# Performance work log

Hardware: AMD Instinct MI355X
Metric: run time of the kernel (lower is better)

The kernel has to match this reference:

```python
import jax, jax.numpy as jnp
import numpy as np

# Event marker constants (PASS/MAP both trigger map writes, STEP triggers step writes)
PASS, MAP, STEP = 0, 1, 2
GRAPH_STEPS = 3
B, T, D, K, V = 64, 12, 256, 256, 512
S = 2 * K  # num_symbols


def gelu(x):
    return jax.nn.gelu(x, approximate=False)  # torch nn.GELU default = exact erf


def mlp2(x, W1, b1, W2, b2):
    return gelu(x @ W1 + b1) @ W2 + b2


def setup_inputs() -> dict:
    key = jax.random.key(0)
    ks = jax.random.split(key, 32)

    def lin(k, fan_in, shape):
        return (jax.random.normal(k, shape, dtype=jnp.float32) / np.float32(np.sqrt(fan_in)))

    return {
        "event_marker": jax.random.randint(ks[0], (B, T), 0, 3),
        "source_idx": jax.random.randint(ks[1], (B, T), 0, S),
        "source_valid": jax.random.randint(ks[2], (B, T), 0, 2),
        "target_symbol_idx": jax.random.randint(ks[3], (B, T), 0, S),
        "target_symbol_valid": jax.random.randint(ks[4], (B, T), 0, 2),
        "target_value_idx": jax.random.randint(ks[5], (B, T), 0, V),
        "target_value_valid": jax.random.randint(ks[6], (B, T), 0, 2),
        "query_idx": jax.random.randint(ks[7], (B,), 0, S),
        "query_valid": jax.random.randint(ks[8], (B,), 0, 2),
        "evidence": jax.random.normal(ks[9], (B, T, D), dtype=jnp.float32),
        "symbol_emb": jax.random.normal(ks[10], (S, D), dtype=jnp.float32) * 0.02,
        "value_emb": jax.random.normal(ks[11], (V, D), dtype=jnp.float32) * 0.02,
        "Wmg1": lin(ks[12], D, (D, D)), "bmg1": jnp.zeros((D,), jnp.float32),
        "Wmg2": lin(ks[13], D, (D, 1)), "bmg2": jnp.zeros((1,), jnp.float32),
        "Wsg1": lin(ks[14], D, (D, D)), "bsg1": jnp.zeros((D,), jnp.float32),
        "Wsg2": lin(ks[15], D, (D, 1)), "bsg2": jnp.zeros((1,), jnp.float32),
        "Wf1": lin(ks[16], 2 * D, (2 * D, D)), "bf1": jnp.zeros((D,), jnp.float32),
        "Wf2": lin(ks[17], D, (D, D)), "bf2": jnp.zeros((D,), jnp.float32),
        "Wo1": lin(ks[18], 2 * D, (2 * D, D)), "bo1": jnp.zeros((D,), jnp.float32),
        "Wo2": lin(ks[19], D, (D, V)), "bo2": jnp.zeros((V,), jnp.float32),
    }


def reference(event_marker, source_idx, source_valid, target_symbol_idx,
              target_symbol_valid, target_value_idx, target_value_valid,
              query_idx, query_valid, evidence, symbol_emb, value_emb,
              Wmg1, bmg1, Wmg2, bmg2, Wsg1, bsg1, Wsg2, bsg2,
              Wf1, bf1, Wf2, bf2, Wo1, bo1, Wo2, bo2):
    f32 = evidence.dtype
    brange = jnp.arange(B)

    # --- TypedGraphMemory.update, applied over T sequential events ---
    # one-hot outer-product write  ==  scatter-add of gated scalar at (b, src, tgt)
    def step(carry, ev):
        map_mem, step_mem = carry
        marker, src, sv, tsym, tsv, tval, tvv, evd = ev
        mg = jax.nn.sigmoid(mlp2(evd, Wmg1, bmg1, Wmg2, bmg2))[:, 0]  # [B]
        sg = jax.nn.sigmoid(mlp2(evd, Wsg1, bsg1, Wsg2, bsg2))[:, 0]  # [B]
        map_mask = (((marker == PASS) | (marker == MAP)) & (sv > 0) & (tvv > 0)).astype(f32)
        step_mask = ((marker == STEP) & (sv > 0) & (tsv > 0)).astype(f32)
        src_c = jnp.clip(src, 0, S - 1)
        tsym_c = jnp.clip(tsym, 0, S - 1)
        tval_c = jnp.clip(tval, 0, V - 1)
        map_mem = map_mem.at[brange, src_c, tval_c].add(mg * map_mask)
        step_mem = step_mem.at[brange, src_c, tsym_c].add(sg * step_mask)
        return (map_mem, step_mem), None

    ev_seq = (event_marker.T, source_idx.T, source_valid.T, target_symbol_idx.T,
              target_symbol_valid.T, target_value_idx.T, target_value_valid.T,
              jnp.swapaxes(evidence, 0, 1))  # time-major
    init = (jnp.zeros((B, S, V), f32), jnp.zeros((B, S, S), f32))
    (map_mem, step_mem), _ = jax.lax.scan(step, init, ev_seq)

    # --- TypedGraphMemory.query_readout ---
    walk = jax.nn.one_hot(jnp.clip(query_idx, 0, S - 1), S, dtype=f32)
    walk = walk * query_valid.astype(f32)[:, None]
    acc_v = jnp.einsum('bs,bsv->bv', walk, map_mem)   # [B,V]
    acc_s = walk @ symbol_emb                         # [B,D]
    for _ in range(GRAPH_STEPS):
        walk = jnp.einsum('bs,bst->bt', walk, step_mem)
        acc_v = acc_v + jnp.einsum('bs,bsv->bv', walk, map_mem)
        acc_s = acc_s + walk @ symbol_emb
    graph_state = jnp.concatenate([acc_s, acc_v @ value_emb], axis=-1)  # [B,2D]
    logits = mlp2(graph_state, Wo1, bo1, Wo2, bo2)      # [B,V]
    feedback = mlp2(graph_state, Wf1, bf1, Wf2, bf2)    # [B,D]
    return logits, feedback
```

## Files before the change

### kernel.cpp

```cpp
#include <hip/hip_runtime.h>
#include <math.h>

#define NB 64
#define NT 12
#define ND 256
#define NS 512
#define NV 512

__device__ __forceinline__ float gelu_exact(float x) {
    return 0.5f * x * (1.0f + erff(x * 0.70710678118654752f));
}
__device__ __forceinline__ float sigmoidf_(float x) {
    return 1.0f / (1.0f + __expf(-x));
}

__global__ __launch_bounds__(512) void k_gates_readout(
    const int* __restrict__ marker, const int* __restrict__ srci,
    const int* __restrict__ srcv, const int* __restrict__ tsymi,
    const int* __restrict__ tsymv, const int* __restrict__ tvali,
    const int* __restrict__ tvalv, const int* __restrict__ qidx,
    const int* __restrict__ qvld,
    const float* __restrict__ evidence,
    const float* __restrict__ symbol_emb, const float* __restrict__ value_emb,
    const float* __restrict__ Wmg1, const float* __restrict__ bmg1,
    const float* __restrict__ Wmg2, const float* __restrict__ bmg2,
    const float* __restrict__ Wsg1, const float* __restrict__ bsg1,
    const float* __restrict__ Wsg2, const float* __restrict__ bsg2,
    float* __restrict__ gs)
{
    const int b = blockIdx.x, tid = threadIdx.x;
    const int g = tid >> 8;
    const int j = tid & 255;
    const int lane = tid & 63, wv = tid >> 6;

    __shared__ float red[8][NT];
    __shared__ float gate_s[2][NT];

    {
        const float* __restrict__ W1 = g ? Wsg1 : Wmg1;
        const float* __restrict__ b1 = g ? bsg1 : bmg1;
        const float* __restrict__ W2 = g ? Wsg2 : Wmg2;
        const float* __restrict__ ev = evidence + b * (NT * ND);

        float h[NT];
        #pragma unroll
        for (int t = 0; t < NT; ++t) h[t] = 0.0f;

        #pragma unroll 8
        for (int i = 0; i < ND; ++i) {
            float w = W1[i * ND + j];
            #pragma unroll
            for (int t = 0; t < NT; ++t) h[t] += ev[t * ND + i] * w;
        }

        const float b1j = b1[j], w2j = W2[j];
        #pragma unroll
        for (int t = 0; t < NT; ++t) {
            float v = gelu_exact(h[t] + b1j) * w2j;
            #pragma unroll
            for (int off = 32; off > 0; off >>= 1) v += __shfl_down(v, off, 64);
            if (lane == 0) red[wv][t] = v;
        }
    }
    __syncthreads();
    if (tid < 24) {
        int gg = tid / NT, tt = tid - gg * NT;
        float s = red[gg * 4 + 0][tt] + red[gg * 4 + 1][tt] +
                  red[gg * 4 + 2][tt] + red[gg * 4 + 3][tt] +
                  (gg ? bsg2[0] : bmg2[0]);
        gate_s[gg][tt] = sigmoidf_(s);
    }

    __shared__ float walk[NS], nxt[NS];
    __shared__ int   esrc[NT], etsym[NT], etval[NT];
    __shared__ float mapw[NT], stepw[NT];
    __shared__ int   sidx[64]; __shared__ float sval[64];
    __shared__ int   vidx[64]; __shared__ float vval[64];
    __shared__ int   scnt, vcnt;

    walk[tid] = 0.f; nxt[tid] = 0.f;
    if (tid == 0) { scnt = 0; vcnt = 0; }
    if (tid >= 256 && tid < 256 + NT) {
        int t = tid - 256;
        int e = b * NT + t;
        int mk = marker[e];
        int sv_ = srcv[e], tsv_ = tsymv[e], tvv_ = tvalv[e];
        esrc[t]  = min(max(srci[e], 0), NS - 1);
        etsym[t] = min(max(tsymi[e], 0), NS - 1);
        etval[t] = min(max(tvali[e], 0), NV - 1);
        mapw[t]  = (((mk == 0) || (mk == 1)) && (sv_ > 0) && (tvv_ > 0)) ? 1.f : 0.f;
        stepw[t] = ((mk == 2) && (sv_ > 0) && (tsv_ > 0)) ? 1.f : 0.f;
    }
    __syncthreads();
    if (tid < NT) {
        mapw[tid]  *= gate_s[0][tid];
        stepw[tid] *= gate_s[1][tid];
    }
    if (tid == 256) {
        int qc = min(max(qidx[b], 0), NS - 1);
        float qv = (float)qvld[b];
        walk[qc] = qv;
        if (qv != 0.f) { sidx[0] = qc; sval[0] = qv; scnt = 1; }
    }
    __syncthreads();
    if (tid < NT) {
        float c = walk[esrc[tid]] * mapw[tid];
        if (c != 0.f) { int k = atomicAdd(&vcnt, 1); vidx[k] = etval[tid]; vval[k] = c; }
    }
    __syncthreads();
    for (int stp = 0; stp < 3; ++stp) {
        if (tid < NT) {
            float c = walk[esrc[tid]] * stepw[tid];
            if (c != 0.f) {
                atomicAdd(&nxt[etsym[tid]], c);
                int k = atomicAdd(&scnt, 1); sidx[k] = etsym[tid]; sval[k] = c;
            }
        }
        __syncthreads();
        { float a = nxt[tid]; walk[tid] = a; nxt[tid] = 0.f; }
        __syncthreads();
        if (tid < NT) {
            float c = walk[esrc[tid]] * mapw[tid];
            if (c != 0.f) { int k = atomicAdd(&vcnt, 1); vidx[k] = etval[tid]; vval[k] = c; }
        }
        __syncthreads();
    }
    const int d = tid & 255;
    const float* __restrict__ emb  = (tid < 256) ? symbol_emb : value_emb;
    const int*   idxl = (tid < 256) ? sidx : vidx;
    const float* vall = (tid < 256) ? sval : vval;
    const int n = (tid < 256) ? scnt : vcnt;
    float acc = 0.f;
    int k = 0;
    for (; k + 4 <= n; k += 4) {
        int   i0 = idxl[k],     i1 = idxl[k + 1], i2 = idxl[k + 2], i3 = idxl[k + 3];
        float w0 = vall[k],     w1 = vall[k + 1], w2 = vall[k + 2], w3 = vall[k + 3];
        float r0 = emb[i0 * ND + d], r1 = emb[i1 * ND + d];
        float r2 = emb[i2 * ND + d], r3 = emb[i3 * ND + d];
        acc += w0 * r0; acc += w1 * r1; acc += w2 * r2; acc += w3 * r3;
    }
    for (; k < n; ++k) acc += vall[k] * emb[idxl[k] * ND + d];
    gs[b * 512 + (tid < 256 ? 0 : 256) + d] = acc;
}

__global__ __launch_bounds__(512) void k_mlp1(
    const float* __restrict__ gs,
    const float* __restrict__ Wo1, const float* __restrict__ bo1,
    const float* __restrict__ Wf1, const float* __restrict__ bf1,
    float* __restrict__ H)
{
    const int blk = blockIdx.x;
    const int m = blk >> 5;
    const int r = blk & 31;
    const int js = r >> 3, bt = r & 7;
    const int tid = threadIdx.x;
    const int lane = tid & 63;
    const int bsub = (tid >> 6) & 3;
    const int ih = tid >> 8;
    const int j = js * 64 + lane;
    const int b0 = bt * 8 + bsub * 2, b1_ = b0 + 1;

    const float* __restrict__ W1   = (m ? Wf1 : Wo1) + ih * 256 * 256;
    const float* __restrict__ bias = m ? bf1 : bo1;
    const float* __restrict__ x0 = gs + b0 * 512 + ih * 256;
    const float* __restrict__ x1 = gs + b1_ * 512 + ih * 256;

    float a0 = 0.f, a1 = 0.f;
    #pragma unroll 8
    for (int i = 0; i < 256; ++i) {
        float w = W1[i * 256 + j];
        a0 += x0[i] * w; a1 += x1[i] * w;
    }
    __shared__ float part[256][2];
    if (ih == 1) { part[tid & 255][0] = a0; part[tid & 255][1] = a1; }
    __syncthreads();
    if (ih == 0) {
        float bj = bias[j];
        H[m * (NB * 256) + b0 * 256 + j]  = gelu_exact(a0 + part[tid][0] + bj);
        H[m * (NB * 256) + b1_ * 256 + j] = gelu_exact(a1 + part[tid][1] + bj);
    }
}

__global__ __launch_bounds__(512) void k_mlp2(
    const float* __restrict__ H,
    const float* __restrict__ Wo2, const float* __restrict__ bo2,
    const float* __restrict__ Wf2, const float* __restrict__ bf2,
    float* __restrict__ out)
{
    const int blk = blockIdx.x;
    const int tid = threadIdx.x;
    const int lane = tid & 63;
    const int bsub = (tid >> 6) & 3;
    const int ih = tid >> 8;
    __shared__ float part[256][2];

    if (blk < 64) {
        const int bt = blk >> 3, vs = blk & 7;
        const int v = vs * 64 + lane;
        const int b0 = bt * 8 + bsub * 2, b1_ = b0 + 1;
        const float* __restrict__ h0 = H + b0 * 256 + ih * 128;
        const float* __restrict__ h1 = H + b1_ * 256 + ih * 128;
        const float* __restrict__ Wp = Wo2 + ih * 128 * 512;
        float a0 = 0.f, a1 = 0.f;
        #pragma unroll 8
        for (int k = 0; k < 128; ++k) {
            float w = Wp[k * 512 + v];
            a0 += h0[k] * w; a1 += h1[k] * w;
        }
        if (ih == 1) { part[tid & 255][0] = a0; part[tid & 255][1] = a1; }
        __syncthreads();
        if (ih == 0) {
            float bv = bo2[v];
            out[b0 * 512 + v]  = a0 + part[tid][0] + bv;
            out[b1_ * 512 + v] = a1 + part[tid][1] + bv;
        }
    } else {
        const int r = blk - 64;
        const int bt = r >> 2, ds = r & 3;
        const int d = ds * 64 + lane;
        const int b0 = bt * 8 + bsub * 2, b1_ = b0 + 1;
        const float* __restrict__ h0 = H + (NB * 256) + b0 * 256 + ih * 128;
        const float* __restrict__ h1 = H + (NB * 256) + b1_ * 256 + ih * 128;
        const float* __restrict__ Wp = Wf2 + ih * 128 * 256;
        float a0 = 0.f, a1 = 0.f;
        #pragma unroll 8
        for (int k = 0; k < 128; ++k) {
            float w = Wp[k * 256 + d];
            a0 += h0[k] * w; a1 += h1[k] * w;
        }
        if (ih == 1) { part[tid & 255][0] = a0; part[tid & 255][1] = a1; }
        __syncthreads();
        if (ih == 0) {
            float bd = bf2[d];
            out[NB * NV + b0 * 256 + d]  = a0 + part[tid][0] + bd;
            out[NB * NV + b1_ * 256 + d] = a1 + part[tid][1] + bd;
        }
    }
}

extern "C" void kernel_launch(void* const* d_in, const int* in_sizes, int n_in,
                              void* d_out, int out_size, void* d_ws, size_t ws_size,
                              hipStream_t stream) {
    const int* event_marker       = (const int*)d_in[0];
    const int* source_idx         = (const int*)d_in[1];
    const int* source_valid       = (const int*)d_in[2];
    const int* target_symbol_idx  = (const int*)d_in[3];
    const int* target_symbol_vld  = (const int*)d_in[4];
    const int* target_value_idx   = (const int*)d_in[5];
    const int* target_value_vld   = (const int*)d_in[6];
    const int* query_idx          = (const int*)d_in[7];
    const int* query_valid        = (const int*)d_in[8];
    const float* evidence   = (const float*)d_in[9];
    const float* symbol_emb = (const float*)d_in[10];
    const float* value_emb  = (const float*)d_in[11];
    const float* Wmg1 = (const float*)d_in[12]; const float* bmg1 = (const float*)d_in[13];
    const float* Wmg2 = (const float*)d_in[14]; const float* bmg2 = (const float*)d_in[15];
    const float* Wsg1 = (const float*)d_in[16]; const float* bsg1 = (const float*)d_in[17];
    const float* Wsg2 = (const float*)d_in[18]; const float* bsg2 = (const float*)d_in[19];
    const float* Wf1  = (const float*)d_in[20]; const float* bf1  = (const float*)d_in[21];
    const float* Wf2  = (const float*)d_in[22]; const float* bf2  = (const float*)d_in[23];
    const float* Wo1  = (const float*)d_in[24]; const float* bo1  = (const float*)d_in[25];
    const float* Wo2  = (const float*)d_in[26]; const float* bo2  = (const float*)d_in[27];

    float* ws = (float*)d_ws;
    float* gs = ws;
    float* H  = ws + 32768;

    k_gates_readout<<<dim3(64), dim3(512), 0, stream>>>(
        event_marker, source_idx, source_valid, target_symbol_idx,
        target_symbol_vld, target_value_idx, target_value_vld,
        query_idx, query_valid, evidence, symbol_emb, value_emb,
        Wmg1, bmg1, Wmg2, bmg2, Wsg1, bsg1, Wsg2, bsg2, gs);
    k_mlp1<<<dim3(64), dim3(512), 0, stream>>>(gs, Wo1, bo1, Wf1, bf1, H);
    k_mlp2<<<dim3(96), dim3(512), 0, stream>>>(H, Wo2, bo2, Wf2, bf2, (float*)d_out);
}
```

Before: 164.0 us.

## Split gate MLP into separate wide-grid kernel before graph readout

Moves the gate MLP computation out of the per-batch readout kernel into its own kernel. The new kernel launches 256 blocks of 1024 threads, split by batch, gate type and time half, with a split-K reduction over the input dimension through shared memory. The aim is to fill far more compute units than the original 64 blocks and shorten the serial dot-product chain per thread. In exchange it adds an extra kernel launch and a global round trip for the gate values.

Result: faster. 155.0 us (-5.5%).

```diff
diff --git a/kernel.cpp b/kernel.cpp
--- a/kernel.cpp
+++ b/kernel.cpp
@@ -14,63 +14,80 @@
     return 1.0f / (1.0f + __expf(-x));
 }
 
-__global__ __launch_bounds__(512) void k_gates_readout(
+__global__ __launch_bounds__(1024) void k_gates(
+    const float* __restrict__ evidence,
+    const float* __restrict__ Wmg1, const float* __restrict__ bmg1,
+    const float* __restrict__ Wmg2, const float* __restrict__ bmg2,
+    const float* __restrict__ Wsg1, const float* __restrict__ bsg1,
+    const float* __restrict__ Wsg2, const float* __restrict__ bsg2,
+    float* __restrict__ gates)
+{
+    const int blk = blockIdx.x;
+    const int b  = blk >> 2;
+    const int g  = (blk >> 1) & 1;
+    const int th = blk & 1;
+    const int t0 = th * 6;
+    const int tid = threadIdx.x;
+    const int j = tid & 255;
+    const int ih = tid >> 8;
+    const int lane = tid & 63, wv = tid >> 6;
+
+    __shared__ float part[3][6][256];
+    __shared__ float red[4][6];
+
+    const float* __restrict__ W1 = g ? Wsg1 : Wmg1;
+    const float* __restrict__ b1 = g ? bsg1 : bmg1;
+    const float* __restrict__ W2 = g ? Wsg2 : Wmg2;
+    const float* __restrict__ b2 = g ? bsg2 : bmg2;
+    const float* __restrict__ ev = evidence + b * (NT * ND) + t0 * ND;
+
+    float h[6];
+    #pragma unroll
+    for (int t = 0; t < 6; ++t) h[t] = 0.0f;
+
+    const int ibase = ih * 64;
+    #pragma unroll 8
+    for (int ii = 0; ii < 64; ++ii) {
+        const int i = ibase + ii;
+        float w = W1[i * ND + j];
+        #pragma unroll
+        for (int t = 0; t < 6; ++t) h[t] += ev[t * ND + i] * w;
+    }
+
+    if (ih > 0) {
+        #pragma unroll
+        for (int t = 0; t < 6; ++t) part[ih - 1][t][j] = h[t];
+    }
+    __syncthreads();
+    if (ih == 0) {
+        const float b1j = b1[j], w2j = W2[j];
+        #pragma unroll
+        for (int t = 0; t < 6; ++t) {
+            float v = gelu_exact(h[t] + part[0][t][j] + part[1][t][j] +
+                                 part[2][t][j] + b1j) * w2j;
+            #pragma unroll
+            for (int off = 32; off > 0; off >>= 1) v += __shfl_down(v, off, 64);
+            if (lane == 0) red[wv][t] = v;
+        }
+    }
+    __syncthreads();
+    if (tid < 6) {
+        float s = red[0][tid] + red[1][tid] + red[2][tid] + red[3][tid] + b2[0];
+        gates[g * (NB * NT) + b * NT + t0 + tid] = sigmoidf_(s);
+    }
+}
+
+__global__ __launch_bounds__(512) void k_readout(
     const int* __restrict__ marker, const int* __restrict__ srci,
     const int* __restrict__ srcv, const int* __restrict__ tsymi,
     const int* __restrict__ tsymv, const int* __restrict__ tvali,
     const int* __restrict__ tvalv, const int* __restrict__ qidx,
     const int* __restrict__ qvld,
-    const float* __restrict__ evidence,
     const float* __restrict__ symbol_emb, const float* __restrict__ value_emb,
-    const float* __restrict__ Wmg1, const float* __restrict__ bmg1,
-    const float* __restrict__ Wmg2, const float* __restrict__ bmg2,
-    const float* __restrict__ Wsg1, const float* __restrict__ bsg1,
-    const float* __restrict__ Wsg2, const float* __restrict__ bsg2,
+    const float* __restrict__ gates,
     float* __restrict__ gs)
 {
     const int b = blockIdx.x, tid = threadIdx.x;
-    const int g = tid >> 8;
-    const int j = tid & 255;
-    const int lane = tid & 63, wv = tid >> 6;
-
-    __shared__ float red[8][NT];
-    __shared__ float gate_s[2][NT];
-
-    {
-        const float* __restrict__ W1 = g ? Wsg1 : Wmg1;
-        const float* __restrict__ b1 = g ? bsg1 : bmg1;
-        const float* __restrict__ W2 = g ? Wsg2 : Wmg2;
-        const float* __restrict__ ev = evidence + b * (NT * ND);
-
-        float h[NT];
-        #pragma unroll
-        for (int t = 0; t < NT; ++t) h[t] = 0.0f;
-
-        #pragma unroll 8
-        for (int i = 0; i < ND; ++i) {
-            float w = W1[i * ND + j];
-            #pragma unroll
-            for (int t = 0; t < NT; ++t) h[t] += ev[t * ND + i] * w;
-        }
-
-        const float b1j = b1[j], w2j = W2[j];
-        #pragma unroll
-        for (int t = 0; t < NT; ++t) {
-            float v = gelu_exact(h[t] + b1j) * w2j;
-            #pragma unroll
-            for (int off = 32; off > 0; off >>= 1) v += __shfl_down(v, off, 64);
-            if (lane == 0) red[wv][t] = v;
-        }
-    }
-    __syncthreads();
-    if (tid < 24) {
-        int gg = tid / NT, tt = tid - gg * NT;
-        float s = red[gg * 4 + 0][tt] + red[gg * 4 + 1][tt] +
-                  red[gg * 4 + 2][tt] + red[gg * 4 + 3][tt] +
-                  (gg ? bsg2[0] : bmg2[0]);
-        gate_s[gg][tt] = sigmoidf_(s);
-    }
-
     __shared__ float walk[NS], nxt[NS];
     __shared__ int   esrc[NT], etsym[NT], etval[NT];
     __shared__ float mapw[NT], stepw[NT];
@@ -80,23 +97,20 @@
 
     walk[tid] = 0.f; nxt[tid] = 0.f;
     if (tid == 0) { scnt = 0; vcnt = 0; }
-    if (tid >= 256 && tid < 256 + NT) {
-        int t = tid - 256;
-        int e = b * NT + t;
+    if (tid < NT) {
+        int e = b * NT + tid;
         int mk = marker[e];
         int sv_ = srcv[e], tsv_ = tsymv[e], tvv_ = tvalv[e];
-        esrc[t]  = min(max(srci[e], 0), NS - 1);
-        etsym[t] = min(max(tsymi[e], 0), NS - 1);
-        etval[t] = min(max(tvali[e], 0), NV - 1);
-        mapw[t]  = (((mk == 0) || (mk == 1)) && (sv_ > 0) && (tvv_ > 0)) ? 1.f : 0.f;
-        stepw[t] = ((mk == 2) && (sv_ > 0) && (tsv_ > 0)) ? 1.f : 0.f;
-    }
-    __syncthreads();
-    if (tid < NT) {
-        mapw[tid]  *= gate_s[0][tid];
-        stepw[tid] *= gate_s[1][tid];
-    }
-    if (tid == 256) {
+        esrc[tid]  = min(max(srci[e], 0), NS - 1);
+        etsym[tid] = min(max(tsymi[e], 0), NS - 1);
+        etval[tid] = min(max(tvali[e], 0), NV - 1);
+        bool mmask = ((mk == 0) || (mk == 1)) && (sv_ > 0) && (tvv_ > 0);
+        bool smask = (mk == 2) && (sv_ > 0) && (tsv_ > 0);
+        mapw[tid]  = mmask ? gates[0 * (NB * NT) + e] : 0.f;
+        stepw[tid] = smask ? gates[1 * (NB * NT) + e] : 0.f;
+    }
+    __syncthreads();
+    if (tid == 0) {
         int qc = min(max(qidx[b], 0), NS - 1);
         float qv = (float)qvld[b];
         walk[qc] = qv;
@@ -262,15 +276,17 @@
     const float* Wo1  = (const float*)d_in[24]; const float* bo1  = (const float*)d_in[25];
     const float* Wo2  = (const float*)d_in[26]; const float* bo2  = (const float*)d_in[27];
 
-    float* ws = (float*)d_ws;
-    float* gs = ws;
-    float* H  = ws + 32768;
-
-    k_gates_readout<<<dim3(64), dim3(512), 0, stream>>>(
+    float* ws    = (float*)d_ws;
+    float* gates = ws;
+    float* gs    = ws + 2048;
+    float* H     = ws + 2048 + 32768;
+
+    k_gates<<<dim3(256), dim3(1024), 0, stream>>>(
+        evidence, Wmg1, bmg1, Wmg2, bmg2, Wsg1, bsg1, Wsg2, bsg2, gates);
+    k_readout<<<dim3(64), dim3(512), 0, stream>>>(
         event_marker, source_idx, source_valid, target_symbol_idx,
         target_symbol_vld, target_value_idx, target_value_vld,
-        query_idx, query_valid, evidence, symbol_emb, value_emb,
-        Wmg1, bmg1, Wmg2, bmg2, Wsg1, bsg1, Wsg2, bsg2, gs);
+        query_idx, query_valid, symbol_emb, value_emb, gates, gs);
     k_mlp1<<<dim3(64), dim3(512), 0, stream>>>(gs, Wo1, bo1, Wf1, bf1, H);
     k_mlp2<<<dim3(96), dim3(512), 0, stream>>>(H, Wo2, bo2, Wf2, bf2, (float*)d_out);
 }
```
